# Performance work log

Hardware: AMD Instinct MI355X
Metric: run time of the kernel (lower is better)

The kernel has to match this reference:

```python
import jax, jax.numpy as jnp
import numpy as np

N_NODES = 100000
N_EDGES = 1600000
D_IN, D_HID, N_CLS = 256, 128, 47


def setup_inputs() -> dict:
    key = jax.random.key(0)
    k = jax.random.split(key, 5)
    x = jax.random.normal(k[0], (N_NODES, D_IN), dtype=jnp.float32)
    edge_index = jax.random.randint(k[1], (2, N_EDGES), 0, N_NODES, dtype=jnp.int64)
    W1 = jax.random.normal(k[2], (D_IN, D_HID), dtype=jnp.float32) * 0.05
    b1 = jnp.zeros((D_HID,), dtype=jnp.float32)
    W2 = jax.random.normal(k[3], (D_HID, N_CLS), dtype=jnp.float32) * 0.05
    b2 = jnp.zeros((N_CLS,), dtype=jnp.float32)
    return {"x": x, "edge_index": edge_index, "W1": W1, "b1": b1, "W2": W2, "b2": b2}


def _gcn_conv(x, W, b, src, dst, norm, n):
    # PyG GCNConv: linear transform, normalized scatter-add aggregation, bias after
    h = x @ W                                   # [N, D_out]
    msg = h[src] * norm[:, None]                # gather over edges [E', D_out]
    agg = jax.ops.segment_sum(msg, dst, num_segments=n)
    return agg + b


def reference(x, edge_index, W1, b1, W2, b2):
    n = x.shape[0]
    loop = jnp.arange(n, dtype=edge_index.dtype)
    src = jnp.concatenate([edge_index[0], loop])  # add self-loops
    dst = jnp.concatenate([edge_index[1], loop])
    # symmetric normalization D^-1/2 (A+I) D^-1/2 (degree = in-degree incl. self-loop)
    deg = jax.ops.segment_sum(jnp.ones_like(dst, dtype=x.dtype), dst, num_segments=n)
    dinv = jnp.where(deg > 0, jax.lax.rsqrt(deg), 0.0)
    norm = dinv[src] * dinv[dst]                 # [E']
    h1 = jax.nn.relu(_gcn_conv(x, W1, b1, src, dst, norm, n))
    # dropout with training=False is identity
    out = _gcn_conv(h1, W2, b2, src, dst, norm, n)
    return out
```

## Files before the change

kernel.cpp:

```cpp
#include <hip/hip_runtime.h>
#include <hip/hip_bf16.h>

#define DIN 256
#define DHID 128
#define NCLS 47
#define BSHIFT 9
#define BNODES 512
#define NPART 256
#define BCAPS 9216

typedef __attribute__((ext_vector_type(8))) short short8;
typedef __attribute__((ext_vector_type(4))) float f32x4;

__device__ __forceinline__ short f2bf(float f) {
    __bf16 b = (__bf16)f;
    return __builtin_bit_cast(short, b);
}
__device__ __forceinline__ float bfu(unsigned int u) {
    return __uint_as_float(u << 16);
}
__device__ __forceinline__ float bfh(unsigned int u) {
    return __uint_as_float(u & 0xffff0000u);
}

__global__ __launch_bounds__(256) void k_hist(const int* __restrict__ dst,
                                              int* __restrict__ ghist,
                                              int E, int NB, int chunk) {
    extern __shared__ int lh[];
    int blk = blockIdx.x, t = threadIdx.x;
    for (int i = t; i < NB; i += 256) lh[i] = 0;
    __syncthreads();
    int lo = blk * chunk, hi = min(E, lo + chunk);
    for (int i = lo + t; i < hi; i += 256)
        atomicAdd(&lh[dst[i] >> BSHIFT], 1);
    __syncthreads();
    for (int i = t; i < NB; i += 256) ghist[blk * NB + i] = lh[i];
}

__global__ __launch_bounds__(256) void k_colscan(const int* __restrict__ ghist,
                                                 int* __restrict__ goff,
                                                 int* __restrict__ btot, int NB) {
    __shared__ int wsum[4];
    int b = blockIdx.x, t = threadIdx.x;
    int v = ghist[t * NB + b];
    int incl = v;
    int lane = t & 63, w = t >> 6;
    #pragma unroll
    for (int off = 1; off < 64; off <<= 1) {
        int u = __shfl_up(incl, off, 64);
        if (lane >= off) incl += u;
    }
    if (lane == 63) wsum[w] = incl;
    __syncthreads();
    int wadd = 0;
    for (int i = 0; i < w; ++i) wadd += wsum[i];
    goff[t * NB + b] = wadd + incl - v;
    if (t == 255) btot[b] = wadd + incl;
}

__device__ __forceinline__ void scan_btot(const int* __restrict__ btot, int NB,
                                          int* lbase, int* wsum) {
    int t = threadIdx.x;
    int v = (t < NB) ? btot[t] : 0;
    int incl = v;
    int lane = t & 63, w = t >> 6;
    #pragma unroll
    for (int off = 1; off < 64; off <<= 1) {
        int u = __shfl_up(incl, off, 64);
        if (lane >= off) incl += u;
    }
    if (lane == 63) wsum[w] = incl;
    __syncthreads();
    int wadd = 0;
    for (int i = 0; i < w; ++i) wadd += wsum[i];
    lbase[t] = wadd + incl - v;
    __syncthreads();
}

__global__ __launch_bounds__(256) void k_scatter(const int* __restrict__ src,
                                                 const int* __restrict__ dst,
                                                 const int* __restrict__ goff,
                                                 const int* __restrict__ btot,
                                                 unsigned int* __restrict__ bbuf,
                                                 int E, int NB, int chunk) {
    __shared__ int lcur[256];
    __shared__ int wsum[4];
    int blk = blockIdx.x, t = threadIdx.x;
    scan_btot(btot, NB, lcur, wsum);
    if (t < NB) lcur[t] += goff[blk * NB + t];
    __syncthreads();
    int lo = blk * chunk, hi = min(E, lo + chunk);
    for (int i = lo + t; i < hi; i += 256) {
        int d = dst[i];
        int b = d >> BSHIFT;
        int pos = atomicAdd(&lcur[b], 1);
        bbuf[pos] = (unsigned int)src[i] | ((unsigned int)(d & (BNODES - 1)) << 17);
    }
}

__global__ __launch_bounds__(256) void k_bsort(const int* __restrict__ btot,
                                               unsigned int* __restrict__ bbuf,
                                               int* __restrict__ degi,
                                               int* __restrict__ beg,
                                               float* __restrict__ dinv, int n, int NB) {
    __shared__ unsigned int stage[BCAPS];
    __shared__ int hist[BNODES];
    __shared__ int cur[BNODES];
    __shared__ int lbase[256];
    __shared__ int wsum[4];

    int b = blockIdx.x, t = threadIdx.x;
    scan_btot(btot, NB, lbase, wsum);
    int cnt = min(btot[b], BCAPS);
    int gbase = lbase[b];
    int node0 = b << BSHIFT;

    if (t < 128) { ((int2*)hist)[t] = (int2){0, 0}; ((int2*)hist)[t + 128] = (int2){0, 0}; }
    __syncthreads();

    for (int i = t; i < cnt; i += 256) {
        unsigned int p = bbuf[gbase + i];
        stage[i] = p;
        atomicAdd(&hist[p >> 17], 1);
    }
    __syncthreads();

    int v0 = hist[2 * t], v1 = hist[2 * t + 1];
    int s = v0 + v1;
    int incl = s;
    int lane = t & 63, w = t >> 6;
    #pragma unroll
    for (int off = 1; off < 64; off <<= 1) {
        int u = __shfl_up(incl, off, 64);
        if (lane >= off) incl += u;
    }
    if (lane == 63) wsum[w] = incl;
    __syncthreads();
    int wadd = 0;
    for (int i = 0; i < w; ++i) wadd += wsum[i];
    int ex = wadd + incl - s;
    cur[2 * t] = ex;
    cur[2 * t + 1] = ex + v0;
    int nodeA = node0 + 2 * t, nodeB = node0 + 2 * t + 1;
    if (nodeA < n) {
        degi[nodeA] = v0;
        beg[nodeA]  = gbase + ex;
        dinv[nodeA] = rsqrtf((float)(v0 + 1));
    }
    if (nodeB < n) {
        degi[nodeB] = v1;
        beg[nodeB]  = gbase + ex + v0;
        dinv[nodeB] = rsqrtf((float)(v1 + 1));
    }
    __syncthreads();

    for (int i = t; i < cnt; i += 256) {
        unsigned int p = stage[i];
        int slot = atomicAdd(&cur[p >> 17], 1);
        bbuf[gbase + slot] = p & 0x1FFFFu;
    }
}

__global__ void k_prepW(const float* __restrict__ W1, const float* __restrict__ W2,
                        short* __restrict__ W1s, short* __restrict__ W2s) {
    int blk = blockIdx.x;
    if (blk < 16) {
        int tid = blk * 256 + threadIdx.x;
        int frag = tid >> 6, lane = tid & 63;
        int kt = frag >> 3, nt = frag & 7;
        int quad = lane >> 4, col = lane & 15;
        #pragma unroll
        for (int j = 0; j < 8; ++j) {
            int k = kt * 32 + quad * 8 + j;
            W1s[(size_t)tid * 8 + j] = f2bf(W1[k * DHID + nt * 16 + col]);
        }
    } else {
        int tid = (blk - 16) * 256 + threadIdx.x;
        int frag = tid >> 6, lane = tid & 63;
        int kt = frag >> 2, nt = frag & 3;
        int quad = lane >> 4, col = lane & 15;
        int c = nt * 16 + col;
        #pragma unroll
        for (int j = 0; j < 8; ++j) {
            int k = kt * 32 + quad * 8 + j;
            float v = (c < NCLS) ? W2[k * NCLS + c] : 0.0f;
            W2s[(size_t)tid * 8 + j] = f2bf(v);
        }
    }
}

__global__ __launch_bounds__(256) void k_gemm1_mfma(const float* __restrict__ x,
                                                    const short* __restrict__ W1s,
                                                    short* __restrict__ hb, int n) {
    __shared__ short lw[32768];
    {
        const uint4* g = (const uint4*)W1s;
        uint4* l = (uint4*)lw;
        for (int i = threadIdx.x; i < 4096; i += 256) l[i] = g[i];
    }
    __syncthreads();

    int wave = threadIdx.x >> 6, lane = threadIdx.x & 63;
    int quad = lane >> 4, lrow = lane & 15;
    long long rowbase = (long long)blockIdx.x * 128 + wave * 32;

    f32x4 acc[2][8];
    #pragma unroll
    for (int rt = 0; rt < 2; ++rt)
        #pragma unroll
        for (int nt = 0; nt < 8; ++nt) acc[rt][nt] = (f32x4){0.f, 0.f, 0.f, 0.f};

    const short8* lf = (const short8*)lw;

    #pragma unroll
    for (int kt = 0; kt < 8; ++kt) {
        int k0 = kt * 32 + quad * 8;
        short8 a[2];
        #pragma unroll
        for (int rt = 0; rt < 2; ++rt) {
            long long row = rowbase + rt * 16 + lrow;
            float4 v0 = {0.f,0.f,0.f,0.f}, v1 = {0.f,0.f,0.f,0.f};
            if (row < n) {
                const float* xp = x + row * DIN + k0;
                v0 = *(const float4*)xp;
                v1 = *(const float4*)(xp + 4);
            }
            short8 av;
            av[0] = f2bf(v0.x); av[1] = f2bf(v0.y); av[2] = f2bf(v0.z); av[3] = f2bf(v0.w);
            av[4] = f2bf(v1.x); av[5] = f2bf(v1.y); av[6] = f2bf(v1.z); av[7] = f2bf(v1.w);
            a[rt] = av;
        }
        #pragma unroll
        for (int nt = 0; nt < 8; ++nt) {
            short8 b = lf[(kt * 8 + nt) * 64 + lane];
            acc[0][nt] = __builtin_amdgcn_mfma_f32_16x16x32_bf16(a[0], b, acc[0][nt], 0, 0, 0);
            acc[1][nt] = __builtin_amdgcn_mfma_f32_16x16x32_bf16(a[1], b, acc[1][nt], 0, 0, 0);
        }
    }
    #pragma unroll
    for (int rt = 0; rt < 2; ++rt)
        #pragma unroll
        for (int nt = 0; nt < 8; ++nt)
            #pragma unroll
            for (int r = 0; r < 4; ++r) {
                long long row = rowbase + rt * 16 + quad * 4 + r;
                if (row < n) hb[row * DHID + nt * 16 + lrow] = f2bf(acc[rt][nt][r]);
            }
}

__global__ void k_gather1(const int* __restrict__ beg, const int* __restrict__ degi,
                          const int* __restrict__ ssrc, const float* __restrict__ dinv,
                          const unsigned int* __restrict__ hu, const float* __restrict__ b1,
                          unsigned int* __restrict__ h1u, int n) {
    int node = blockIdx.x * 4 + (threadIdx.x >> 6);
    int t = threadIdx.x & 63;
    if (node >= n) return;
    int cnt = degi[node];
    int bg  = beg[node];
    float ax = 0.f, ay = 0.f;
    int k = 0;
    for (; k + 8 <= cnt; k += 8) {
        int s[8]; float dv[8]; unsigned int u[8];
        #pragma unroll
        for (int j = 0; j < 8; ++j) s[j] = ssrc[bg + k + j];
        #pragma unroll
        for (int j = 0; j < 8; ++j) { dv[j] = dinv[s[j]]; u[j] = hu[(size_t)s[j] * 64 + t]; }
        #pragma unroll
        for (int j = 0; j < 8; ++j) { ax += dv[j] * bfu(u[j]); ay += dv[j] * bfh(u[j]); }
    }
    for (; k + 4 <= cnt; k += 4) {
        int s[4]; float dv[4]; unsigned int u[4];
        #pragma unroll
        for (int j = 0; j < 4; ++j) s[j] = ssrc[bg + k + j];
        #pragma unroll
        for (int j = 0; j < 4; ++j) { dv[j] = dinv[s[j]]; u[j] = hu[(size_t)s[j] * 64 + t]; }
        #pragma unroll
        for (int j = 0; j < 4; ++j) { ax += dv[j] * bfu(u[j]); ay += dv[j] * bfh(u[j]); }
    }
    for (; k < cnt; ++k) {
        int s = ssrc[bg + k];
        float ds = dinv[s];
        unsigned int u = hu[(size_t)s * 64 + t];
        ax += ds * bfu(u);
        ay += ds * bfh(u);
    }
    float di = dinv[node];
    unsigned int us = hu[(size_t)node * 64 + t];
    float2 bb = ((const float2*)b1)[t];
    float vx = di * ax + bfu(us) * di * di + bb.x;
    float vy = di * ay + bfh(us) * di * di + bb.y;
    vx = vx > 0.f ? vx : 0.f;
    vy = vy > 0.f ? vy : 0.f;
    unsigned int o = (unsigned int)(unsigned short)f2bf(vx)
                   | ((unsigned int)(unsigned short)f2bf(vy) << 16);
    h1u[(size_t)node * 64 + t] = o;
}

__global__ __launch_bounds__(256) void k_gemm2_mfma(const short* __restrict__ h1b,
                                                    const short* __restrict__ W2s,
                                                    short* __restrict__ h2b, int n) {
    __shared__ short lw[8192];
    {
        const uint4* g = (const uint4*)W2s;
        uint4* l = (uint4*)lw;
        for (int i = threadIdx.x; i < 1024; i += 256) l[i] = g[i];
    }
    __syncthreads();

    int wave = threadIdx.x >> 6, lane = threadIdx.x & 63;
    int quad = lane >> 4, lrow = lane & 15;
    long long row0 = (long long)blockIdx.x * 64 + wave * 16;

    f32x4 acc[4];
    #pragma unroll
    for (int nt = 0; nt < 4; ++nt) acc[nt] = (f32x4){0.f, 0.f, 0.f, 0.f};

    const short8* lf = (const short8*)lw;

    #pragma unroll
    for (int kt = 0; kt < 4; ++kt) {
        long long row = row0 + lrow;
        short8 a = (short8){0,0,0,0,0,0,0,0};
        if (row < n) a = *(const short8*)(h1b + row * DHID + kt * 32 + quad * 8);
        #pragma unroll
        for (int nt = 0; nt < 4; ++nt)
            acc[nt] = __builtin_amdgcn_mfma_f32_16x16x32_bf16(a, lf[(kt * 4 + nt) * 64 + lane], acc[nt], 0, 0, 0);
    }
    #pragma unroll
    for (int nt = 0; nt < 4; ++nt)
        #pragma unroll
        for (int r = 0; r < 4; ++r) {
            long long row = row0 + quad * 4 + r;
            if (row < n) h2b[row * 64 + nt * 16 + lrow] = f2bf(acc[nt][r]);
        }
}

__global__ void k_gather2(const int* __restrict__ beg, const int* __restrict__ degi,
                          const int* __restrict__ ssrc, const float* __restrict__ dinv,
                          const unsigned short* __restrict__ h2b, const float* __restrict__ b2,
                          float* __restrict__ out, int n) {
    int node = blockIdx.x * 4 + (threadIdx.x >> 6);
    int t = threadIdx.x & 63;
    if (node >= n) return;
    int cnt = degi[node];
    int bg  = beg[node];
    float acc = 0.f;
    int k = 0;
    for (; k + 8 <= cnt; k += 8) {
        int s[8]; float dv[8]; unsigned int u[8];
        #pragma unroll
        for (int j = 0; j < 8; ++j) s[j] = ssrc[bg + k + j];
        #pragma unroll
        for (int j = 0; j < 8; ++j) { dv[j] = dinv[s[j]]; u[j] = h2b[(size_t)s[j] * 64 + t]; }
        #pragma unroll
        for (int j = 0; j < 8; ++j) acc += dv[j] * bfu(u[j]);
    }
    for (; k + 4 <= cnt; k += 4) {
        int s[4]; float dv[4]; unsigned int u[4];
        #pragma unroll
        for (int j = 0; j < 4; ++j) s[j] = ssrc[bg + k + j];
        #pragma unroll
        for (int j = 0; j < 4; ++j) { dv[j] = dinv[s[j]]; u[j] = h2b[(size_t)s[j] * 64 + t]; }
        #pragma unroll
        for (int j = 0; j < 4; ++j) acc += dv[j] * bfu(u[j]);
    }
    for (; k < cnt; ++k) {
        int s = ssrc[bg + k];
        acc += dinv[s] * bfu((unsigned int)h2b[(size_t)s * 64 + t]);
    }
    if (t < NCLS) {
        float di = dinv[node];
        float self = bfu((unsigned int)h2b[(size_t)node * 64 + t]);
        out[(size_t)node * NCLS + t] = di * acc + self * di * di + b2[t];
    }
}

extern "C" void kernel_launch(void* const* d_in, const int* in_sizes, int n_in,
                              void* d_out, int out_size, void* d_ws, size_t ws_size,
                              hipStream_t stream) {
    const float* x  = (const float*)d_in[0];
    const int*   ei = (const int*)d_in[1];
    const float* W1 = (const float*)d_in[2];
    const float* b1 = (const float*)d_in[3];
    const float* W2 = (const float*)d_in[4];
    const float* b2 = (const float*)d_in[5];

    const int n = in_sizes[0] / DIN;
    const int E = in_sizes[1] / 2;
    const int* src = ei;
    const int* dst = ei + E;
    float* out = (float*)d_out;

    const int NB = (n + BNODES - 1) >> BSHIFT;
    const int chunk = (E + NPART - 1) / NPART;

    char* w = (char*)d_ws;
    int*   ghist = (int*)w;                    w += (size_t)NPART * NB * 4;
    int*   goff  = (int*)w;                    w += (size_t)NPART * NB * 4;
    int*   btot  = (int*)w;                    w += ((size_t)NB * 4 + 15) & ~15ull;
    int*   degi  = (int*)w;                    w += (size_t)n * 4;
    int*   beg   = (int*)w;                    w += (size_t)n * 4;
    float* dinv  = (float*)w;                  w += (size_t)n * 4;
    short* W1s   = (short*)w;                  w += (size_t)32768 * 2;
    short* W2s   = (short*)w;                  w += (size_t)8192 * 2;
    unsigned int* bbuf = (unsigned int*)w;     w += (size_t)E * 4;
    short* hb    = (short*)w;                  w += (size_t)n * DHID * 2;
    short* h1b   = (short*)w;                  w += (size_t)n * DHID * 2;
    short* h2b   = (short*)w;                  w += (size_t)n * 64 * 2;

    k_prepW<<<20, 256, 0, stream>>>(W1, W2, W1s, W2s);
    k_hist<<<NPART, 256, NB * 4, stream>>>(dst, ghist, E, NB, chunk);
    k_colscan<<<NB, 256, 0, stream>>>(ghist, goff, btot, NB);
    k_scatter<<<NPART, 256, 0, stream>>>(src, dst, goff, btot, bbuf, E, NB, chunk);
    k_bsort<<<NB, 256, 0, stream>>>(btot, bbuf, degi, beg, dinv, n, NB);

    k_gemm1_mfma<<<(n + 127) / 128, 256, 0, stream>>>(x, W1s, hb, n);
    k_gather1<<<(n + 3) / 4, 256, 0, stream>>>(beg, degi, (const int*)bbuf, dinv,
                                               (const unsigned int*)hb, b1,
                                               (unsigned int*)h1b, n);

    k_gemm2_mfma<<<(n + 63) / 64, 256, 0, stream>>>(h1b, W2s, h2b, n);
    k_gather2<<<(n + 3) / 4, 256, 0, stream>>>(beg, degi, (const int*)bbuf, dinv,
                                               (const unsigned short*)h2b, b2, out, n);
}
```

Measured before the change: 410.4 us.

## Stage scatter through LDS for coalesced bucket writes and merge weight prep into histogram

The scatter kernel now computes per-block local bucket offsets, sorts each chunk's edges into shared memory by bucket, then writes them out in bucket-contiguous order so global stores are mostly contiguous instead of random. The weight conversion kernel is folded into the histogram kernel as extra blocks, removing one launch. This costs about 51KB of LDS per scatter block, which lowers occupancy, and assumes each chunk holds at most CHUNKE edges and that NB is at most 256.

```diff
diff --git a/kernel.cpp b/kernel.cpp
--- a/kernel.cpp
+++ b/kernel.cpp
@@ -8,6 +8,7 @@
 #define BNODES 512
 #define NPART 256
 #define BCAPS 9216
+#define CHUNKE 6400
 
 typedef __attribute__((ext_vector_type(8))) short short8;
 typedef __attribute__((ext_vector_type(4))) float f32x4;
@@ -23,18 +24,47 @@
     return __uint_as_float(u & 0xffff0000u);
 }
 
-__global__ __launch_bounds__(256) void k_hist(const int* __restrict__ dst,
-                                              int* __restrict__ ghist,
-                                              int E, int NB, int chunk) {
-    extern __shared__ int lh[];
+__global__ __launch_bounds__(256) void k_prep_hist(const float* __restrict__ W1,
+                                                   const float* __restrict__ W2,
+                                                   short* __restrict__ W1s,
+                                                   short* __restrict__ W2s,
+                                                   const int* __restrict__ dst,
+                                                   int* __restrict__ ghist,
+                                                   int E, int NB, int chunk) {
+    __shared__ int lh[256];
     int blk = blockIdx.x, t = threadIdx.x;
-    for (int i = t; i < NB; i += 256) lh[i] = 0;
-    __syncthreads();
-    int lo = blk * chunk, hi = min(E, lo + chunk);
-    for (int i = lo + t; i < hi; i += 256)
-        atomicAdd(&lh[dst[i] >> BSHIFT], 1);
-    __syncthreads();
-    for (int i = t; i < NB; i += 256) ghist[blk * NB + i] = lh[i];
+    if (blk < 16) {
+        int tid = blk * 256 + t;
+        int frag = tid >> 6, lane = tid & 63;
+        int kt = frag >> 3, nt = frag & 7;
+        int quad = lane >> 4, col = lane & 15;
+        #pragma unroll
+        for (int j = 0; j < 8; ++j) {
+            int k = kt * 32 + quad * 8 + j;
+            W1s[(size_t)tid * 8 + j] = f2bf(W1[k * DHID + nt * 16 + col]);
+        }
+    } else if (blk < 20) {
+        int tid = (blk - 16) * 256 + t;
+        int frag = tid >> 6, lane = tid & 63;
+        int kt = frag >> 2, nt = frag & 3;
+        int quad = lane >> 4, col = lane & 15;
+        int c = nt * 16 + col;
+        #pragma unroll
+        for (int j = 0; j < 8; ++j) {
+            int k = kt * 32 + quad * 8 + j;
+            float v = (c < NCLS) ? W2[k * NCLS + c] : 0.0f;
+            W2s[(size_t)tid * 8 + j] = f2bf(v);
+        }
+    } else {
+        int p = blk - 20;
+        for (int i = t; i < NB; i += 256) lh[i] = 0;
+        __syncthreads();
+        int lo = p * chunk, hi = min(E, lo + chunk);
+        for (int i = lo + t; i < hi; i += 256)
+            atomicAdd(&lh[dst[i] >> BSHIFT], 1);
+        __syncthreads();
+        for (int i = t; i < NB; i += 256) ghist[p * NB + i] = lh[i];
+    }
 }
 
 __global__ __launch_bounds__(256) void k_colscan(const int* __restrict__ ghist,
@@ -79,23 +109,51 @@
 
 __global__ __launch_bounds__(256) void k_scatter(const int* __restrict__ src,
                                                  const int* __restrict__ dst,
+                                                 const int* __restrict__ ghist,
                                                  const int* __restrict__ goff,
                                                  const int* __restrict__ btot,
                                                  unsigned int* __restrict__ bbuf,
                                                  int E, int NB, int chunk) {
+    __shared__ unsigned int stage[CHUNKE];
+    __shared__ int sdest[CHUNKE];
     __shared__ int lcur[256];
+    __shared__ int gdst[256];
     __shared__ int wsum[4];
+
     int blk = blockIdx.x, t = threadIdx.x;
-    scan_btot(btot, NB, lcur, wsum);
-    if (t < NB) lcur[t] += goff[blk * NB + t];
-    __syncthreads();
-    int lo = blk * chunk, hi = min(E, lo + chunk);
+
+    scan_btot(btot, NB, gdst, wsum);
+
+    int v = (t < NB) ? ghist[blk * NB + t] : 0;
+    {
+        int incl = v;
+        int lane = t & 63, w = t >> 6;
+        #pragma unroll
+        for (int off = 1; off < 64; off <<= 1) {
+            int u = __shfl_up(incl, off, 64);
+            if (lane >= off) incl += u;
+        }
+        if (lane == 63) wsum[w] = incl;
+        __syncthreads();
+        int wadd = 0;
+        for (int i = 0; i < w; ++i) wadd += wsum[i];
+        int ex = wadd + incl - v;
+        lcur[t] = ex;
+        if (t < NB) gdst[t] += goff[blk * NB + t] - ex;
+    }
+    __syncthreads();
+
+    int lo = blk * chunk, hi = min(E, lo + chunk), cnt = hi - lo;
     for (int i = lo + t; i < hi; i += 256) {
         int d = dst[i];
         int b = d >> BSHIFT;
-        int pos = atomicAdd(&lcur[b], 1);
-        bbuf[pos] = (unsigned int)src[i] | ((unsigned int)(d & (BNODES - 1)) << 17);
-    }
+        int slot = atomicAdd(&lcur[b], 1);
+        stage[slot] = (unsigned int)src[i] | ((unsigned int)(d & (BNODES - 1)) << 17);
+        sdest[slot] = gdst[b] + slot;
+    }
+    __syncthreads();
+    for (int i = t; i < cnt; i += 256)
+        bbuf[sdest[i]] = stage[i];
 }
 
 __global__ __launch_bounds__(256) void k_bsort(const int* __restrict__ btot,
@@ -158,34 +216,6 @@
         unsigned int p = stage[i];
         int slot = atomicAdd(&cur[p >> 17], 1);
         bbuf[gbase + slot] = p & 0x1FFFFu;
-    }
-}
-
-__global__ void k_prepW(const float* __restrict__ W1, const float* __restrict__ W2,
-                        short* __restrict__ W1s, short* __restrict__ W2s) {
-    int blk = blockIdx.x;
-    if (blk < 16) {
-        int tid = blk * 256 + threadIdx.x;
-        int frag = tid >> 6, lane = tid & 63;
-        int kt = frag >> 3, nt = frag & 7;
-        int quad = lane >> 4, col = lane & 15;
-        #pragma unroll
-        for (int j = 0; j < 8; ++j) {
-            int k = kt * 32 + quad * 8 + j;
-            W1s[(size_t)tid * 8 + j] = f2bf(W1[k * DHID + nt * 16 + col]);
-        }
-    } else {
-        int tid = (blk - 16) * 256 + threadIdx.x;
-        int frag = tid >> 6, lane = tid & 63;
-        int kt = frag >> 2, nt = frag & 3;
-        int quad = lane >> 4, col = lane & 15;
-        int c = nt * 16 + col;
-        #pragma unroll
-        for (int j = 0; j < 8; ++j) {
-            int k = kt * 32 + quad * 8 + j;
-            float v = (c < NCLS) ? W2[k * NCLS + c] : 0.0f;
-            W2s[(size_t)tid * 8 + j] = f2bf(v);
-        }
     }
 }
 
@@ -408,10 +438,9 @@
     short* h1b   = (short*)w;                  w += (size_t)n * DHID * 2;
     short* h2b   = (short*)w;                  w += (size_t)n * 64 * 2;
 
-    k_prepW<<<20, 256, 0, stream>>>(W1, W2, W1s, W2s);
-    k_hist<<<NPART, 256, NB * 4, stream>>>(dst, ghist, E, NB, chunk);
+    k_prep_hist<<<20 + NPART, 256, 0, stream>>>(W1, W2, W1s, W2s, dst, ghist, E, NB, chunk);
     k_colscan<<<NB, 256, 0, stream>>>(ghist, goff, btot, NB);
-    k_scatter<<<NPART, 256, 0, stream>>>(src, dst, goff, btot, bbuf, E, NB, chunk);
+    k_scatter<<<NPART, 256, 0, stream>>>(src, dst, ghist, goff, btot, bbuf, E, NB, chunk);
     k_bsort<<<NB, 256, 0, stream>>>(btot, bbuf, degi, beg, dinv, n, NB);
 
     k_gemm1_mfma<<<(n + 127) / 128, 256, 0, stream>>>(x, W1s, hb, n);
```

Result: no change. 404.3 us (-1.5%).
